# Optimization experiments

Measured on AMD Instinct MI355X. Metric: run time of the kernel, lower is better.

The kernel has to match this reference:

```python
import jax, jax.numpy as jnp
import numpy as np

N = 50000      # nodes
E = 800000     # edges
D = 128        # d_model
H = 8          # heads
DH = D // H    # head dim
FF = 512       # dim_ff
NB = 32        # degree buckets
EPS = 1e-5


def _ln(x, g, b):
    mu = jnp.mean(x, axis=-1, keepdims=True)
    var = jnp.mean((x - mu) ** 2, axis=-1, keepdims=True)
    return (x - mu) * jax.lax.rsqrt(var + EPS) * g + b


def setup_inputs() -> dict:
    key = jax.random.key(0)
    ks = jax.random.split(key, 12)
    s = 0.02
    return {
        'x': jax.random.normal(ks[0], (N, D), jnp.float32),
        'row': jnp.sort(jax.random.randint(ks[1], (E,), 0, N, jnp.int32)),
        'col': jax.random.randint(ks[2], (E,), 0, N, jnp.int32),
        'deg_bucket': jax.random.randint(ks[3], (N,), 0, NB, jnp.int32),
        'Wq': jax.random.normal(ks[4], (D, D), jnp.float32) * s,
        'bq': jnp.zeros((D,), jnp.float32),
        'Wk': jax.random.normal(ks[5], (D, D), jnp.float32) * s,
        'bk': jnp.zeros((D,), jnp.float32),
        'Wv': jax.random.normal(ks[6], (D, D), jnp.float32) * s,
        'bv': jnp.zeros((D,), jnp.float32),
        'Wo': jax.random.normal(ks[7], (D, D), jnp.float32) * s,
        'bo': jnp.zeros((D,), jnp.float32),
        'emb': jax.random.normal(ks[8], (NB, H), jnp.float32) * s,
        'ln1_g': jnp.ones((D,), jnp.float32), 'ln1_b': jnp.zeros((D,), jnp.float32),
        'ln2_g': jnp.ones((D,), jnp.float32), 'ln2_b': jnp.zeros((D,), jnp.float32),
        'W1': jax.random.normal(ks[9], (D, FF), jnp.float32) * s,
        'b1': jnp.zeros((FF,), jnp.float32),
        'W2': jax.random.normal(ks[10], (FF, D), jnp.float32) * s,
        'b2': jnp.zeros((D,), jnp.float32),
    }


def reference(x, row, col, deg_bucket, Wq, bq, Wk, bk, Wv, bv, Wo, bo, emb,
              ln1_g, ln1_b, ln2_g, ln2_b, W1, b1, W2, b2):
    scale = DH ** (-0.5)
    Q = (x @ Wq + bq).reshape(N, H, DH)
    K = (x @ Wk + bk).reshape(N, H, DH)
    V = (x @ Wv + bv).reshape(N, H, DH)
    # edge-wise QK dot products: [E, H]
    scores = jnp.einsum('ehd,ehd->eh', Q[row], K[col]) * scale
    scores = scores + emb[deg_bucket[row]] + emb[deg_bucket[col]]
    # segment softmax over destination node `row`
    max_s = jax.ops.segment_max(scores, row, num_segments=N, indices_are_sorted=True)
    exp_s = jnp.exp(scores - max_s[row])
    sum_s = jax.ops.segment_sum(exp_s, row, num_segments=N, indices_are_sorted=True)
    alpha = exp_s / jnp.maximum(sum_s[row], 1e-12)
    # scatter-weighted aggregation of V[col]: [N, H, DH]
    agg = jax.ops.segment_sum(alpha[..., None] * V[col], row, num_segments=N,
                              indices_are_sorted=True)
    out = agg.reshape(N, D) @ Wo + bo
    h = _ln(x + out, ln1_g, ln1_b)
    ffo = jax.nn.gelu(h @ W1 + b1, approximate=False) @ W2 + b2
    return _ln(h + ffo, ln2_g, ln2_b)
```

## Files before the change

kernel.cpp:

```cpp
#include <hip/hip_runtime.h>
#include <math.h>

#define NN 50000
#define NE 800000
#define DM 128
#define NH 8
#define FF 512
#define NBLK 391
#define NBLK64 782

#define PB_X    6250
#define PB_WT   192
#define PB_RP   196
#define PB_EMB  1563
#define PB_TOT  (PB_X + PB_WT + PB_RP + PB_EMB)

typedef __attribute__((ext_vector_type(8))) short bf16x8;
typedef __attribute__((ext_vector_type(4))) float f32x4;
typedef __attribute__((ext_vector_type(2))) float f32x2;

__device__ __forceinline__ short f2bf(float f) {
    union { float f; unsigned u; } v; v.f = f;
    unsigned r = v.u + 0x7fff + ((v.u >> 16) & 1);
    return (short)(r >> 16);
}
__device__ __forceinline__ float bf2f(short s) {
    union { unsigned u; float f; } v; v.u = ((unsigned)(unsigned short)s) << 16;
    return v.f;
}
__device__ __forceinline__ unsigned char f2fp8(float f) {
    int p = __builtin_amdgcn_cvt_pk_fp8_f32(f, f, 0, false);
    return (unsigned char)(p & 0xff);
}

__device__ __forceinline__ float gelu_f(float x) {
    float u = x * (0.7978845608f + 0.0356774081f * x * x);
    float t = 1.f - 2.f / (__expf(2.f * u) + 1.f);
    return 0.5f * x * (1.f + t);
}

__device__ __forceinline__ void gload16(const void* g, void* l) {
    __builtin_amdgcn_global_load_lds(
        (const __attribute__((address_space(1))) void*)g,
        (__attribute__((address_space(3))) void*)l, 16, 0, 0);
}

__device__ __forceinline__ void stage_tile(const short* __restrict__ src, int row0,
                                           int maxrow, int ld, int col0,
                                           short* sm) {
    const int tid = threadIdx.x;
    const int w = tid >> 6, l = tid & 63;
    const int p = l & 15;
    #pragma unroll
    for (int j = 0; j < 8; ++j) {
        int lr = w * 32 + j * 4 + (l >> 4);
        int gr = row0 + lr; gr = gr > maxrow ? maxrow : gr;
        int s = p ^ (lr & 7);
        const short* g = src + (size_t)gr * ld + col0 + s * 8;
        gload16(g, sm + (w * 32 + j * 4) * 128);
    }
}

template <int R>
__device__ __forceinline__ void stage_tile_f8(const unsigned char* __restrict__ src,
                                              int row0, int maxrow, int ld, int col0,
                                              unsigned char* sm) {
    const int tid = threadIdx.x;
    const int w = tid >> 6, l = tid & 63;
    const int p = l & 7;
    const int rsub = l >> 3;
    #pragma unroll
    for (int j = 0; j < (R >> 5); ++j) {
        int lr = w * (R >> 2) + j * 8 + rsub;
        int gr = row0 + lr; gr = gr > maxrow ? maxrow : gr;
        int g = p ^ (lr & 7);
        const unsigned char* gp = src + (size_t)gr * ld + col0 + g * 16;
        gload16(gp, sm + (w * (R >> 2) + j * 8) * 128);
    }
}

__device__ __forceinline__ bf16x8 frag_ld(const short* sm, int outer, int slot) {
    return *(const bf16x8*)(sm + outer * 128 + ((slot ^ (outer & 7)) << 3));
}

__device__ __forceinline__ long frag_ld_f8(const unsigned char* sm, int outer, int slot) {
    return *(const long*)(sm + outer * 128 +
                          (((slot >> 1) ^ (outer & 7)) << 4) + ((slot & 1) << 3));
}

__device__ __forceinline__ void mfma_tile(const short* sA, const short* sB,
                                          int wm, int wn, int lane,
                                          f32x4 acc[4][4]) {
    const int l15 = lane & 15, l4 = lane >> 4;
    #pragma unroll
    for (int ks = 0; ks < 4; ++ks) {
        bf16x8 a[4], b[4];
        int slot = ks * 4 + l4;
        #pragma unroll
        for (int f = 0; f < 4; ++f) a[f] = frag_ld(sA, wm * 64 + f * 16 + l15, slot);
        #pragma unroll
        for (int f = 0; f < 4; ++f) b[f] = frag_ld(sB, wn * 64 + f * 16 + l15, slot);
        #pragma unroll
        for (int fm = 0; fm < 4; ++fm)
            #pragma unroll
            for (int fn = 0; fn < 4; ++fn)
                acc[fm][fn] = __builtin_amdgcn_mfma_f32_16x16x32_bf16(
                    a[fm], b[fn], acc[fm][fn], 0, 0, 0);
    }
}

__device__ __forceinline__ void mfma_tile64_f8(const unsigned char* sA,
                                               const unsigned char* sB,
                                               int wm, int wn, int lane,
                                               f32x4 acc[2][4]) {
    const int l15 = lane & 15, l4 = lane >> 4;
    #pragma unroll
    for (int ks = 0; ks < 4; ++ks) {
        long a[2], b[4];
        int slot = ks * 4 + l4;
        #pragma unroll
        for (int f = 0; f < 2; ++f) a[f] = frag_ld_f8(sA, wm * 32 + f * 16 + l15, slot);
        #pragma unroll
        for (int f = 0; f < 4; ++f) b[f] = frag_ld_f8(sB, wn * 64 + f * 16 + l15, slot);
        #pragma unroll
        for (int fm = 0; fm < 2; ++fm)
            #pragma unroll
            for (int fn = 0; fn < 4; ++fn)
                acc[fm][fn] = __builtin_amdgcn_mfma_f32_16x16x32_fp8_fp8(
                    a[fm], b[fn], acc[fm][fn], 0, 0, 0);
    }
}

__global__ __launch_bounds__(256) void k_prep(
    const float* __restrict__ x, short* __restrict__ xb,
    const float* __restrict__ Wq, const float* __restrict__ Wk,
    const float* __restrict__ Wv, const float* __restrict__ Wo,
    const float* __restrict__ W1, const float* __restrict__ W2,
    short* __restrict__ wts,
    unsigned char* __restrict__ w1f8, unsigned char* __restrict__ w2f8,
    const int* __restrict__ row, int* __restrict__ rowptr,
    const int* __restrict__ db, const float* __restrict__ emb,
    float* __restrict__ embn)
{
    int bid = blockIdx.x;
    const int tid = threadIdx.x;

    if (bid < PB_X) {
        int i = bid * 256 + tid;
        if (i < NN * DM / 4) {
            float4 v = ((const float4*)x)[i];
            ((short4*)xb)[i] = make_short4(f2bf(v.x), f2bf(v.y), f2bf(v.z), f2bf(v.w));
        }
        return;
    }
    bid -= PB_X;
    if (bid < PB_WT) {
        const float* W; int K, N, bx, by;
        short* Wt = nullptr; unsigned char* Wf8 = nullptr;
        if (bid < 64) {
            int wsel = bid >> 4, rel = bid & 15;
            W = wsel == 0 ? Wq : wsel == 1 ? Wk : wsel == 2 ? Wv : Wo;
            Wt = wts + wsel * 16384; K = 128; N = 128; bx = rel & 3; by = rel >> 2;
        } else if (bid < 128) {
            int rel = bid - 64;
            W = W1; Wf8 = w1f8; K = 128; N = 512; bx = rel & 15; by = rel >> 4;
        } else {
            int rel = bid - 128;
            W = W2; Wf8 = w2f8; K = 512; N = 128; bx = rel & 3; by = rel >> 2;
        }
        __shared__ float t[32][33];
        int n0 = bx * 32, k0 = by * 32;
        int r = tid >> 3, c4 = (tid & 7) * 4;
        float4 v = *(const float4*)(W + (size_t)(k0 + r) * N + n0 + c4);
        t[r][c4 + 0] = v.x; t[r][c4 + 1] = v.y; t[r][c4 + 2] = v.z; t[r][c4 + 3] = v.w;
        __syncthreads();
        if (Wt) {
            short4 o = make_short4(f2bf(t[c4 + 0][r]), f2bf(t[c4 + 1][r]),
                                   f2bf(t[c4 + 2][r]), f2bf(t[c4 + 3][r]));
            *(short4*)(Wt + (size_t)(n0 + r) * K + k0 + c4) = o;
        } else {
            uchar4 o = make_uchar4(f2fp8(16.f * t[c4 + 0][r]), f2fp8(16.f * t[c4 + 1][r]),
                                   f2fp8(16.f * t[c4 + 2][r]), f2fp8(16.f * t[c4 + 3][r]));
            *(uchar4*)(Wf8 + (size_t)(n0 + r) * K + k0 + c4) = o;
        }
        return;
    }
    bid -= PB_WT;
    if (bid < PB_RP) {
        int n = bid * 256 + tid;
        if (n > NN) return;
        int lo = 0, hi = NE;
        while (lo < hi) {
            int mid = (lo + hi) >> 1;
            if (row[mid] < n) lo = mid + 1; else hi = mid;
        }
        rowptr[n] = lo;
        return;
    }
    bid -= PB_RP;
    {
        int i = bid * 256 + tid;
        if (i < NN * NH) embn[i] = emb[db[i >> 3] * NH + (i & 7)];
    }
}

__global__ __launch_bounds__(256) void k_gemm_qkv(
    const short* __restrict__ xb, const short* __restrict__ Wt,
    const float* __restrict__ bq, const float* __restrict__ bk,
    const float* __restrict__ bv,
    short* __restrict__ Qb, unsigned char* __restrict__ Kf8,
    unsigned char* __restrict__ Vf8)
{
    __shared__ short sm[2 * 16384];
    const int tid = threadIdx.x, lane = tid & 63, wid = tid >> 6;
    const int wm = wid >> 1, wn = wid & 1;
    const int r0 = blockIdx.x * 128;

    stage_tile(xb, r0, NN - 1, 128, 0, sm);
    #pragma unroll
    for (int m = 0; m < 3; ++m) {
        if (m) __syncthreads();
        stage_tile(Wt + m * 16384, 0, 127, 128, 0, sm + 16384);
        __syncthreads();
        f32x4 acc[4][4];
        #pragma unroll
        for (int i = 0; i < 4; ++i)
            #pragma unroll
            for (int j = 0; j < 4; ++j)
                acc[i][j] = (f32x4){0.f, 0.f, 0.f, 0.f};
        mfma_tile(sm, sm + 16384, wm, wn, lane, acc);

        const float* bias = m == 0 ? bq : (m == 1 ? bk : bv);
        #pragma unroll
        for (int fn = 0; fn < 4; ++fn) {
            int col = wn * 64 + fn * 16 + (lane & 15);
            float bc = bias[col];
            #pragma unroll
            for (int fm = 0; fm < 4; ++fm) {
                int rowb = r0 + wm * 64 + fm * 16 + (lane >> 4) * 4;
                #pragma unroll
                for (int rr = 0; rr < 4; ++rr) {
                    int gr = rowb + rr;
                    if (gr < NN) {
                        float v = acc[fm][fn][rr] + bc;
                        if (m == 0)
                            Qb[(size_t)gr * DM + col] = f2bf(v);
                        else if (m == 1)
                            Kf8[(size_t)gr * DM + col] = f2fp8(v);
                        else
                            Vf8[(size_t)gr * DM + col] = f2fp8(v);
                    }
                }
            }
        }
    }
}

__global__ __launch_bounds__(256) void k_attn_wave(
    const short* __restrict__ Qb, const unsigned char* __restrict__ Kf8,
    const unsigned char* __restrict__ Vf8, const int* __restrict__ col,
    const int* __restrict__ rowptr, const float* __restrict__ embn,
    short* __restrict__ aggb)
{
    const int lane = threadIdx.x & 63;
    const int n = blockIdx.x * 4 + (threadIdx.x >> 6);
    const int e0 = rowptr[n], e1 = rowptr[n + 1];
    const int s = lane >> 3, h = lane & 7;
    const int h2 = lane >> 3;

    f32x2 qf2[8];
    {
        const bf16x8* qp = (const bf16x8*)(Qb + (size_t)n * DM + h * 16);
        bf16x8 q0 = qp[0], q1 = qp[1];
        #pragma unroll
        for (int j = 0; j < 4; ++j) {
            qf2[j] = (f32x2){bf2f(q0[2 * j]), bf2f(q0[2 * j + 1])};
            qf2[4 + j] = (f32x2){bf2f(q1[2 * j]), bf2f(q1[2 * j + 1])};
        }
    }
    const float embr = embn[(size_t)n * NH + h];

    float m = -INFINITY, l = 0.f;
    f32x2 accv = (f32x2){0.f, 0.f};

    for (int c0 = e0; c0 < e1; c0 += 16) {
        int ea = c0 + s, eb = c0 + 8 + s;
        bool va = ea < e1, vb = eb < e1;
        int ca = col[va ? ea : e1 - 1];
        int cb = col[vb ? eb : e1 - 1];

        int4 kwa = *(const int4*)(Kf8 + (size_t)ca * DM + h * 16);
        int4 kwb = *(const int4*)(Kf8 + (size_t)cb * DM + h * 16);
        float ema = embn[(size_t)ca * NH + h];
        float emB = embn[(size_t)cb * NH + h];

        int nv = e1 - c0; nv = nv > 16 ? 16 : nv;
        unsigned short vv[16];
        #pragma unroll
        for (int j = 0; j < 8; ++j) {
            int cj = __shfl(ca, j * 8);
            vv[j] = (j < nv) ? *(const unsigned short*)(Vf8 + (size_t)cj * DM + lane * 2) : 0;
        }
        #pragma unroll
        for (int j = 0; j < 8; ++j) {
            int cj = __shfl(cb, j * 8);
            vv[8 + j] = (8 + j < nv) ? *(const unsigned short*)(Vf8 + (size_t)cj * DM + lane * 2) : 0;
        }

        f32x2 da2 = (f32x2){0.f, 0.f}, db2 = (f32x2){0.f, 0.f};
        {
            int ka[4] = {kwa.x, kwa.y, kwa.z, kwa.w};
            int kb[4] = {kwb.x, kwb.y, kwb.z, kwb.w};
            #pragma unroll
            for (int w = 0; w < 4; ++w) {
                f32x2 alo = __builtin_amdgcn_cvt_pk_f32_fp8(ka[w], false);
                f32x2 ahi = __builtin_amdgcn_cvt_pk_f32_fp8(ka[w], true);
                f32x2 blo = __builtin_amdgcn_cvt_pk_f32_fp8(kb[w], false);
                f32x2 bhi = __builtin_amdgcn_cvt_pk_f32_fp8(kb[w], true);
                da2 += qf2[2 * w] * alo + qf2[2 * w + 1] * ahi;
                db2 += qf2[2 * w] * blo + qf2[2 * w + 1] * bhi;
            }
        }
        float da = da2[0] + da2[1];
        float dbv = db2[0] + db2[1];
        float sa = va ? da * 0.25f + embr + ema : -INFINITY;
        float sb = vb ? dbv * 0.25f + embr + emB : -INFINITY;

        float mc = fmaxf(sa, sb);
        mc = fmaxf(mc, __shfl_xor(mc, 8));
        mc = fmaxf(mc, __shfl_xor(mc, 16));
        mc = fmaxf(mc, __shfl_xor(mc, 32));
        float mn = fmaxf(m, mc);
        float f = __expf(m - mn);
        m = mn;
        float pa = __expf(sa - mn);
        float pb = __expf(sb - mn);
        float ps = pa + pb;
        ps += __shfl_xor(ps, 8);
        ps += __shfl_xor(ps, 16);
        ps += __shfl_xor(ps, 32);
        l = l * f + ps;

        float fr = __shfl(f, h2);
        accv *= (f32x2){fr, fr};
        #pragma unroll
        for (int j = 0; j < 8; ++j) {
            float pj = __shfl(pa, j * 8 + h2);
            f32x2 vd = __builtin_amdgcn_cvt_pk_f32_fp8((int)vv[j], false);
            accv += (f32x2){pj, pj} * vd;
        }
        #pragma unroll
        for (int j = 0; j < 8; ++j) {
            float pj = __shfl(pb, j * 8 + h2);
            f32x2 vd = __builtin_amdgcn_cvt_pk_f32_fp8((int)vv[8 + j], false);
            accv += (f32x2){pj, pj} * vd;
        }
    }
    float la = __shfl(l, h2);
    la = fmaxf(la, 1e-12f);
    unsigned o = ((unsigned)(unsigned short)f2bf(accv[0] / la)) |
                 (((unsigned)(unsigned short)f2bf(accv[1] / la)) << 16);
    *(unsigned*)(aggb + (size_t)n * DM + lane * 2) = o;
}

__global__ __launch_bounds__(256) void k_gemm_ln1(
    const short* __restrict__ aggb, const short* __restrict__ Wot,
    const float* __restrict__ bo, const short* __restrict__ xbr,
    const float* __restrict__ g, const float* __restrict__ b,
    short* __restrict__ hb, unsigned char* __restrict__ hb8)
{
    __shared__ union { short ab[2 * 16384]; float hs[128 * 129]; } u;
    __shared__ float mu[128], rsd[128];
    const int tid = threadIdx.x, lane = tid & 63, wid = tid >> 6;
    const int wm = wid >> 1, wn = wid & 1;
    const int r0 = blockIdx.x * 128;

    stage_tile(aggb, r0, NN - 1, 128, 0, u.ab);
    stage_tile(Wot, 0, 127, 128, 0, u.ab + 16384);
    __syncthreads();

    f32x4 acc[4][4];
    #pragma unroll
    for (int i = 0; i < 4; ++i)
        #pragma unroll
        for (int j = 0; j < 4; ++j) acc[i][j] = (f32x4){0.f, 0.f, 0.f, 0.f};
    mfma_tile(u.ab, u.ab + 16384, wm, wn, lane, acc);
    __syncthreads();

    #pragma unroll
    for (int fn = 0; fn < 4; ++fn) {
        int col = wn * 64 + fn * 16 + (lane & 15);
        float bc = bo[col];
        #pragma unroll
        for (int fm = 0; fm < 4; ++fm) {
            int rowb = wm * 64 + fm * 16 + (lane >> 4) * 4;
            #pragma unroll
            for (int rr = 0; rr < 4; ++rr) {
                int r_ = rowb + rr, gr = r0 + r_;
                float xr = (gr < NN) ? bf2f(xbr[(size_t)gr * DM + col]) : 0.f;
                u.hs[r_ * 129 + col] = acc[fm][fn][rr] + bc + xr;
            }
        }
    }
    __syncthreads();

    {
        int rrow = tid >> 1, half = tid & 1;
        float s = 0.f, q = 0.f;
        #pragma unroll 8
        for (int c = 0; c < 64; ++c) {
            float v = u.hs[rrow * 129 + half * 64 + c];
            s += v; q += v * v;
        }
        s += __shfl_xor(s, 1);
        q += __shfl_xor(q, 1);
        float m = s * (1.f / DM);
        float var = q * (1.f / DM) - m * m;
        if (half == 0) { mu[rrow] = m; rsd[rrow] = rsqrtf(var + 1e-5f); }
    }
    __syncthreads();

    for (int i = 0; i < 64; ++i) {
        int idx = i * 256 + tid;
        int rrow = idx >> 7, c = idx & 127;
        int gr = r0 + rrow;
        if (gr < NN) {
            float v = (u.hs[rrow * 129 + c] - mu[rrow]) * rsd[rrow] * g[c] + b[c];
            hb[(size_t)gr * DM + c] = f2bf(v);
            hb8[(size_t)gr * DM + c] = f2fp8(v);
        }
    }
}

__global__ __launch_bounds__(256) void k_ffn_fused(
    const unsigned char* __restrict__ hb8, const unsigned char* __restrict__ W1f8,
    const float* __restrict__ b1, const unsigned char* __restrict__ W2f8,
    const float* __restrict__ b2, const short* __restrict__ hb,
    const float* __restrict__ g, const float* __restrict__ bb,
    float* __restrict__ out)
{
    extern __shared__ char smraw[];
    unsigned char* A = (unsigned char*)smraw;
    unsigned char* B = A + 8192;
    unsigned char* C = B + 16384;
    float* hs = (float*)smraw;
    __shared__ float mu[64], rsd[64];

    const int tid = threadIdx.x, lane = tid & 63, wid = tid >> 6;
    const int wm = wid >> 1, wn = wid & 1;
    const int l15 = lane & 15, l4 = lane >> 4;
    const int r0 = blockIdx.x * 64;

    f32x4 acc2[2][4];
    #pragma unroll
    for (int i = 0; i < 2; ++i)
        #pragma unroll
        for (int j = 0; j < 4; ++j) acc2[i][j] = (f32x4){0.f, 0.f, 0.f, 0.f};

    stage_tile_f8<64>(hb8, r0, NN - 1, 128, 0, A);

    for (int kc = 0; kc < 4; ++kc) {
        if (kc) __syncthreads();
        stage_tile_f8<128>(W1f8, kc * 128, FF - 1, 128, 0, B);
        __syncthreads();

        f32x4 accf[2][4];
        #pragma unroll
        for (int i = 0; i < 2; ++i)
            #pragma unroll
            for (int j = 0; j < 4; ++j) accf[i][j] = (f32x4){0.f, 0.f, 0.f, 0.f};
        mfma_tile64_f8(A, B, wm, wn, lane, accf);

        #pragma unroll
        for (int fn = 0; fn < 4; ++fn) {
            int nloc = wn * 64 + fn * 16 + l15;
            float bc = b1[kc * 128 + nloc];
            #pragma unroll
            for (int fm = 0; fm < 2; ++fm) {
                int rowb = wm * 32 + fm * 16 + l4 * 4;
                #pragma unroll
                for (int rr = 0; rr < 4; ++rr) {
                    int row = rowb + rr;
                    float v = 16.f * gelu_f(accf[fm][fn][rr] * 0.0625f + bc);
                    C[row * 128 + ((((nloc >> 4) ^ (row & 7)) << 4) | (nloc & 15))]
                        = f2fp8(v);
                }
            }
        }
        __syncthreads();
        stage_tile_f8<128>(W2f8, 0, 127, 512, kc * 128, B);
        __syncthreads();
        mfma_tile64_f8(C, B, wm, wn, lane, acc2);
    }
    __syncthreads();

    #pragma unroll
    for (int fn = 0; fn < 4; ++fn) {
        int col = wn * 64 + fn * 16 + l15;
        float bc = b2[col];
        #pragma unroll
        for (int fm = 0; fm < 2; ++fm) {
            int rowb = wm * 32 + fm * 16 + l4 * 4;
            #pragma unroll
            for (int rr = 0; rr < 4; ++rr) {
                int r_ = rowb + rr, gr = r0 + r_;
                int cr = gr < NN ? gr : NN - 1;
                float hr = bf2f(hb[(size_t)cr * DM + col]);
                hs[r_ * 129 + col] = acc2[fm][fn][rr] * (1.f / 256.f) + bc + hr;
            }
        }
    }
    __syncthreads();

    {
        int rrow = tid >> 2, q = tid & 3;
        float s = 0.f, qq = 0.f;
        #pragma unroll 8
        for (int c = 0; c < 32; ++c) {
            float v = hs[rrow * 129 + q * 32 + c];
            s += v; qq += v * v;
        }
        s += __shfl_xor(s, 1);  qq += __shfl_xor(qq, 1);
        s += __shfl_xor(s, 2);  qq += __shfl_xor(qq, 2);
        float m = s * (1.f / DM);
        float var = qq * (1.f / DM) - m * m;
        if (q == 0) { mu[rrow] = m; rsd[rrow] = rsqrtf(var + 1e-5f); }
    }
    __syncthreads();

    for (int i = 0; i < 32; ++i) {
        int idx = i * 256 + tid;
        int rrow = idx >> 7, c = idx & 127;
        int gr = r0 + rrow;
        if (gr < NN)
            out[(size_t)gr * DM + c] =
                (hs[rrow * 129 + c] - mu[rrow]) * rsd[rrow] * g[c] + bb[c];
    }
}

extern "C" void kernel_launch(void* const* d_in, const int* in_sizes, int n_in,
                              void* d_out, int out_size, void* d_ws, size_t ws_size,
                              hipStream_t stream) {
    const float* x   = (const float*)d_in[0];
    const int* row   = (const int*)d_in[1];
    const int* col   = (const int*)d_in[2];
    const int* db    = (const int*)d_in[3];
    const float* Wq  = (const float*)d_in[4];
    const float* bq  = (const float*)d_in[5];
    const float* Wk  = (const float*)d_in[6];
    const float* bk  = (const float*)d_in[7];
    const float* Wv  = (const float*)d_in[8];
    const float* bv  = (const float*)d_in[9];
    const float* Wo  = (const float*)d_in[10];
    const float* bo  = (const float*)d_in[11];
    const float* emb = (const float*)d_in[12];
    const float* g1  = (const float*)d_in[13];
    const float* b1n = (const float*)d_in[14];
    const float* g2  = (const float*)d_in[15];
    const float* b2n = (const float*)d_in[16];
    const float* W1  = (const float*)d_in[17];
    const float* b1  = (const float*)d_in[18];
    const float* W2  = (const float*)d_in[19];
    const float* b2  = (const float*)d_in[20];

    char* W = (char*)d_ws;
    float* embn          = (float*)(W + 0);
    unsigned char* Kf8   = (unsigned char*)(W + 1600000);
    unsigned char* Vf8   = (unsigned char*)(W + 8000000);
    short* aggb   = (short*)(W + 25600000);
    short* xb     = (short*)(W + 38400000);
    short* Qb     = (short*)(W + 51200000);
    short* hb     = (short*)(W + 51200000);
    unsigned char* hb8 = (unsigned char*)(W + 76800000);
    short* wts    = (short*)(W + 89600000);
    unsigned char* w1f8 = (unsigned char*)(W + 89731072);
    unsigned char* w2f8 = (unsigned char*)(W + 89796608);
    int* rowptr   = (int*)(W + 89862144);

    k_prep<<<PB_TOT, 256, 0, stream>>>(x, xb, Wq, Wk, Wv, Wo, W1, W2, wts,
                                       w1f8, w2f8, row, rowptr, db, emb, embn);
    k_gemm_qkv<<<NBLK, 256, 0, stream>>>(xb, wts, bq, bk, bv, Qb, Kf8, Vf8);
    k_attn_wave<<<NN / 4, 256, 0, stream>>>(Qb, Kf8, Vf8, col, rowptr, embn, aggb);
    k_gemm_ln1<<<NBLK, 256, 0, stream>>>(aggb, wts + 49152, bo, xb, g1, b1n, hb, hb8);
    k_ffn_fused<<<NBLK64, 256, 33024, stream>>>(hb8, w1f8, b1, w2f8, b2, hb,
                                                g2, b2n, (float*)d_out);
}
```

Baseline: 181.1 us.

## Switch QKV and output-projection GEMMs from bf16 to fp8 operands

Converts x, the Q/K/V/O weights and the attention aggregate to fp8 (scaled by 16) and runs the QKV and Wo GEMMs with fp8 MFMA instead of bf16, rescaling the accumulators afterwards. This halves the bytes staged into LDS and written for the aggregate, and uses the faster fp8 matrix instructions. In exchange, k_prep does extra work to write an fp8 copy of x, and the lower precision loses accuracy, especially for unscaled x values in e4m3.

```diff
diff --git a/kernel.cpp b/kernel.cpp
--- a/kernel.cpp
+++ b/kernel.cpp
@@ -43,22 +43,6 @@
     __builtin_amdgcn_global_load_lds(
         (const __attribute__((address_space(1))) void*)g,
         (__attribute__((address_space(3))) void*)l, 16, 0, 0);
-}
-
-__device__ __forceinline__ void stage_tile(const short* __restrict__ src, int row0,
-                                           int maxrow, int ld, int col0,
-                                           short* sm) {
-    const int tid = threadIdx.x;
-    const int w = tid >> 6, l = tid & 63;
-    const int p = l & 15;
-    #pragma unroll
-    for (int j = 0; j < 8; ++j) {
-        int lr = w * 32 + j * 4 + (l >> 4);
-        int gr = row0 + lr; gr = gr > maxrow ? maxrow : gr;
-        int s = p ^ (lr & 7);
-        const short* g = src + (size_t)gr * ld + col0 + s * 8;
-        gload16(g, sm + (w * 32 + j * 4) * 128);
-    }
 }
 
 template <int R>
@@ -79,32 +63,29 @@
     }
 }
 
-__device__ __forceinline__ bf16x8 frag_ld(const short* sm, int outer, int slot) {
-    return *(const bf16x8*)(sm + outer * 128 + ((slot ^ (outer & 7)) << 3));
-}
-
 __device__ __forceinline__ long frag_ld_f8(const unsigned char* sm, int outer, int slot) {
     return *(const long*)(sm + outer * 128 +
                           (((slot >> 1) ^ (outer & 7)) << 4) + ((slot & 1) << 3));
 }
 
-__device__ __forceinline__ void mfma_tile(const short* sA, const short* sB,
-                                          int wm, int wn, int lane,
-                                          f32x4 acc[4][4]) {
+__device__ __forceinline__ void mfma_tile128_f8(const unsigned char* sA,
+                                                const unsigned char* sB,
+                                                int wm, int wn, int lane,
+                                                f32x4 acc[4][4]) {
     const int l15 = lane & 15, l4 = lane >> 4;
     #pragma unroll
     for (int ks = 0; ks < 4; ++ks) {
-        bf16x8 a[4], b[4];
+        long a[4], b[4];
         int slot = ks * 4 + l4;
         #pragma unroll
-        for (int f = 0; f < 4; ++f) a[f] = frag_ld(sA, wm * 64 + f * 16 + l15, slot);
-        #pragma unroll
-        for (int f = 0; f < 4; ++f) b[f] = frag_ld(sB, wn * 64 + f * 16 + l15, slot);
+        for (int f = 0; f < 4; ++f) a[f] = frag_ld_f8(sA, wm * 64 + f * 16 + l15, slot);
+        #pragma unroll
+        for (int f = 0; f < 4; ++f) b[f] = frag_ld_f8(sB, wn * 64 + f * 16 + l15, slot);
         #pragma unroll
         for (int fm = 0; fm < 4; ++fm)
             #pragma unroll
             for (int fn = 0; fn < 4; ++fn)
-                acc[fm][fn] = __builtin_amdgcn_mfma_f32_16x16x32_bf16(
+                acc[fm][fn] = __builtin_amdgcn_mfma_f32_16x16x32_fp8_fp8(
                     a[fm], b[fn], acc[fm][fn], 0, 0, 0);
     }
 }
@@ -133,10 +114,11 @@
 
 __global__ __launch_bounds__(256) void k_prep(
     const float* __restrict__ x, short* __restrict__ xb,
+    unsigned char* __restrict__ xb8,
     const float* __restrict__ Wq, const float* __restrict__ Wk,
     const float* __restrict__ Wv, const float* __restrict__ Wo,
     const float* __restrict__ W1, const float* __restrict__ W2,
-    short* __restrict__ wts,
+    unsigned char* __restrict__ wqkvo,
     unsigned char* __restrict__ w1f8, unsigned char* __restrict__ w2f8,
     const int* __restrict__ row, int* __restrict__ rowptr,
     const int* __restrict__ db, const float* __restrict__ emb,
@@ -150,17 +132,18 @@
         if (i < NN * DM / 4) {
             float4 v = ((const float4*)x)[i];
             ((short4*)xb)[i] = make_short4(f2bf(v.x), f2bf(v.y), f2bf(v.z), f2bf(v.w));
+            ((uchar4*)xb8)[i] = make_uchar4(f2fp8(v.x), f2fp8(v.y), f2fp8(v.z), f2fp8(v.w));
         }
         return;
     }
     bid -= PB_X;
     if (bid < PB_WT) {
         const float* W; int K, N, bx, by;
-        short* Wt = nullptr; unsigned char* Wf8 = nullptr;
+        unsigned char* Wf8;
         if (bid < 64) {
             int wsel = bid >> 4, rel = bid & 15;
             W = wsel == 0 ? Wq : wsel == 1 ? Wk : wsel == 2 ? Wv : Wo;
-            Wt = wts + wsel * 16384; K = 128; N = 128; bx = rel & 3; by = rel >> 2;
+            Wf8 = wqkvo + wsel * 16384; K = 128; N = 128; bx = rel & 3; by = rel >> 2;
         } else if (bid < 128) {
             int rel = bid - 64;
             W = W1; Wf8 = w1f8; K = 128; N = 512; bx = rel & 15; by = rel >> 4;
@@ -174,15 +157,9 @@
         float4 v = *(const float4*)(W + (size_t)(k0 + r) * N + n0 + c4);
         t[r][c4 + 0] = v.x; t[r][c4 + 1] = v.y; t[r][c4 + 2] = v.z; t[r][c4 + 3] = v.w;
         __syncthreads();
-        if (Wt) {
-            short4 o = make_short4(f2bf(t[c4 + 0][r]), f2bf(t[c4 + 1][r]),
-                                   f2bf(t[c4 + 2][r]), f2bf(t[c4 + 3][r]));
-            *(short4*)(Wt + (size_t)(n0 + r) * K + k0 + c4) = o;
-        } else {
-            uchar4 o = make_uchar4(f2fp8(16.f * t[c4 + 0][r]), f2fp8(16.f * t[c4 + 1][r]),
-                                   f2fp8(16.f * t[c4 + 2][r]), f2fp8(16.f * t[c4 + 3][r]));
-            *(uchar4*)(Wf8 + (size_t)(n0 + r) * K + k0 + c4) = o;
-        }
+        uchar4 o = make_uchar4(f2fp8(16.f * t[c4 + 0][r]), f2fp8(16.f * t[c4 + 1][r]),
+                               f2fp8(16.f * t[c4 + 2][r]), f2fp8(16.f * t[c4 + 3][r]));
+        *(uchar4*)(Wf8 + (size_t)(n0 + r) * K + k0 + c4) = o;
         return;
     }
     bid -= PB_WT;
@@ -205,22 +182,23 @@
 }
 
 __global__ __launch_bounds__(256) void k_gemm_qkv(
-    const short* __restrict__ xb, const short* __restrict__ Wt,
+    const unsigned char* __restrict__ xb8, const unsigned char* __restrict__ wqkvo,
     const float* __restrict__ bq, const float* __restrict__ bk,
     const float* __restrict__ bv,
     short* __restrict__ Qb, unsigned char* __restrict__ Kf8,
     unsigned char* __restrict__ Vf8)
 {
-    __shared__ short sm[2 * 16384];
+    __shared__ unsigned char smA[16384];
+    __shared__ unsigned char smB[16384];
     const int tid = threadIdx.x, lane = tid & 63, wid = tid >> 6;
     const int wm = wid >> 1, wn = wid & 1;
     const int r0 = blockIdx.x * 128;
 
-    stage_tile(xb, r0, NN - 1, 128, 0, sm);
+    stage_tile_f8<128>(xb8, r0, NN - 1, 128, 0, smA);
     #pragma unroll
     for (int m = 0; m < 3; ++m) {
         if (m) __syncthreads();
-        stage_tile(Wt + m * 16384, 0, 127, 128, 0, sm + 16384);
+        stage_tile_f8<128>(wqkvo + m * 16384, 0, 127, 128, 0, smB);
         __syncthreads();
         f32x4 acc[4][4];
         #pragma unroll
@@ -228,7 +206,7 @@
             #pragma unroll
             for (int j = 0; j < 4; ++j)
                 acc[i][j] = (f32x4){0.f, 0.f, 0.f, 0.f};
-        mfma_tile(sm, sm + 16384, wm, wn, lane, acc);
+        mfma_tile128_f8(smA, smB, wm, wn, lane, acc);
 
         const float* bias = m == 0 ? bq : (m == 1 ? bk : bv);
         #pragma unroll
@@ -242,7 +220,7 @@
                 for (int rr = 0; rr < 4; ++rr) {
                     int gr = rowb + rr;
                     if (gr < NN) {
-                        float v = acc[fm][fn][rr] + bc;
+                        float v = acc[fm][fn][rr] * 0.0625f + bc;
                         if (m == 0)
                             Qb[(size_t)gr * DM + col] = f2bf(v);
                         else if (m == 1)
@@ -260,7 +238,7 @@
     const short* __restrict__ Qb, const unsigned char* __restrict__ Kf8,
     const unsigned char* __restrict__ Vf8, const int* __restrict__ col,
     const int* __restrict__ rowptr, const float* __restrict__ embn,
-    short* __restrict__ aggb)
+    unsigned char* __restrict__ agg8)
 {
     const int lane = threadIdx.x & 63;
     const int n = blockIdx.x * 4 + (threadIdx.x >> 6);
@@ -358,25 +336,28 @@
     }
     float la = __shfl(l, h2);
     la = fmaxf(la, 1e-12f);
-    unsigned o = ((unsigned)(unsigned short)f2bf(accv[0] / la)) |
-                 (((unsigned)(unsigned short)f2bf(accv[1] / la)) << 16);
-    *(unsigned*)(aggb + (size_t)n * DM + lane * 2) = o;
+    int p = __builtin_amdgcn_cvt_pk_fp8_f32(16.f * accv[0] / la,
+                                            16.f * accv[1] / la, 0, false);
+    *(unsigned short*)(agg8 + (size_t)n * DM + lane * 2) = (unsigned short)p;
 }
 
 __global__ __launch_bounds__(256) void k_gemm_ln1(
-    const short* __restrict__ aggb, const short* __restrict__ Wot,
+    const unsigned char* __restrict__ agg8, const unsigned char* __restrict__ Wof8,
     const float* __restrict__ bo, const short* __restrict__ xbr,
     const float* __restrict__ g, const float* __restrict__ b,
     short* __restrict__ hb, unsigned char* __restrict__ hb8)
 {
-    __shared__ union { short ab[2 * 16384]; float hs[128 * 129]; } u;
+    __shared__ union {
+        struct { unsigned char A[16384]; unsigned char B[16384]; } s;
+        float hs[128 * 129];
+    } u;
     __shared__ float mu[128], rsd[128];
     const int tid = threadIdx.x, lane = tid & 63, wid = tid >> 6;
     const int wm = wid >> 1, wn = wid & 1;
     const int r0 = blockIdx.x * 128;
 
-    stage_tile(aggb, r0, NN - 1, 128, 0, u.ab);
-    stage_tile(Wot, 0, 127, 128, 0, u.ab + 16384);
+    stage_tile_f8<128>(agg8, r0, NN - 1, 128, 0, u.s.A);
+    stage_tile_f8<128>(Wof8, 0, 127, 128, 0, u.s.B);
     __syncthreads();
 
     f32x4 acc[4][4];
@@ -384,7 +365,7 @@
     for (int i = 0; i < 4; ++i)
         #pragma unroll
         for (int j = 0; j < 4; ++j) acc[i][j] = (f32x4){0.f, 0.f, 0.f, 0.f};
-    mfma_tile(u.ab, u.ab + 16384, wm, wn, lane, acc);
+    mfma_tile128_f8(u.s.A, u.s.B, wm, wn, lane, acc);
     __syncthreads();
 
     #pragma unroll
@@ -398,7 +379,7 @@
             for (int rr = 0; rr < 4; ++rr) {
                 int r_ = rowb + rr, gr = r0 + r_;
                 float xr = (gr < NN) ? bf2f(xbr[(size_t)gr * DM + col]) : 0.f;
-                u.hs[r_ * 129 + col] = acc[fm][fn][rr] + bc + xr;
+                u.hs[r_ * 129 + col] = acc[fm][fn][rr] * (1.f / 256.f) + bc + xr;
             }
         }
     }
@@ -567,21 +548,22 @@
     float* embn          = (float*)(W + 0);
     unsigned char* Kf8   = (unsigned char*)(W + 1600000);
     unsigned char* Vf8   = (unsigned char*)(W + 8000000);
-    short* aggb   = (short*)(W + 25600000);
+    unsigned char* xb8   = (unsigned char*)(W + 14400000);
+    unsigned char* agg8  = (unsigned char*)(W + 20800000);
     short* xb     = (short*)(W + 38400000);
     short* Qb     = (short*)(W + 51200000);
     short* hb     = (short*)(W + 51200000);
     unsigned char* hb8 = (unsigned char*)(W + 76800000);
-    short* wts    = (short*)(W + 89600000);
-    unsigned char* w1f8 = (unsigned char*)(W + 89731072);
-    unsigned char* w2f8 = (unsigned char*)(W + 89796608);
-    int* rowptr   = (int*)(W + 89862144);
-
-    k_prep<<<PB_TOT, 256, 0, stream>>>(x, xb, Wq, Wk, Wv, Wo, W1, W2, wts,
-                                       w1f8, w2f8, row, rowptr, db, emb, embn);
-    k_gemm_qkv<<<NBLK, 256, 0, stream>>>(xb, wts, bq, bk, bv, Qb, Kf8, Vf8);
-    k_attn_wave<<<NN / 4, 256, 0, stream>>>(Qb, Kf8, Vf8, col, rowptr, embn, aggb);
-    k_gemm_ln1<<<NBLK, 256, 0, stream>>>(aggb, wts + 49152, bo, xb, g1, b1n, hb, hb8);
+    unsigned char* wqkvo = (unsigned char*)(W + 89600000);
+    unsigned char* w1f8  = (unsigned char*)(W + 89665536);
+    unsigned char* w2f8  = (unsigned char*)(W + 89731072);
+    int* rowptr   = (int*)(W + 89796608);
+
+    k_prep<<<PB_TOT, 256, 0, stream>>>(x, xb, xb8, Wq, Wk, Wv, Wo, W1, W2,
+                                       wqkvo, w1f8, w2f8, row, rowptr, db, emb, embn);
+    k_gemm_qkv<<<NBLK, 256, 0, stream>>>(xb8, wqkvo, bq, bk, bv, Qb, Kf8, Vf8);
+    k_attn_wave<<<NN / 4, 256, 0, stream>>>(Qb, Kf8, Vf8, col, rowptr, embn, agg8);
+    k_gemm_ln1<<<NBLK, 256, 0, stream>>>(agg8, wqkvo + 49152, bo, xb, g1, b1n, hb, hb8);
     k_ffn_fused<<<NBLK64, 256, 33024, stream>>>(hb8, w1f8, b1, w2f8, b2, hb,
                                                 g2, b2n, (float*)d_out);
 }
```

Result: no change. 179.3 us (-0.9%).
